# Optimization experiments

Hardware: AMD Instinct MI355X
Metric: run time of the kernel (lower is better)

The kernel has to match this reference:

```python
import jax, jax.numpy as jnp
import numpy as np

L1 = 0.5  # link length 1 (module-level torch.Tensor([0.5]))
L2 = 0.5  # link length 2
SIZE = 8388608
N_MULTS = 1  # len(mul_approx_func_arr)
EPS = 1e-6


def setup_inputs() -> dict:
    key = jax.random.key(0)
    k1, k2 = jax.random.split(key)
    inp = jax.random.normal(k1, (1, SIZE, 2), dtype=jnp.float32)
    # nn.Parameter init: np.tile([1,1,1,1]*100, (n_mults,1)) -> all 100.0
    weight = jnp.ones((N_MULTS, 4), dtype=jnp.float32) * 100.0
    return {"input": inp, "weight": weight}


def _st_clamp(a, lo, hi):
    # value = clamp(a, lo, hi); gradient = identity (matches torch data-swap + hardtanh)
    return a + jax.lax.stop_gradient(jnp.clip(a, lo, hi) - a)


def _forward(inp, weight):
    x = inp[0, :, 0]  # (SIZE,)
    y = inp[0, :, 1]  # (SIZE,)
    outs = []
    for ii in range(weight.shape[0]):  # loop over small fixed n_mults
        w = weight[ii]
        # QuantizeGrad: round+clamp forward, straight-through gradient
        c = w + jax.lax.stop_gradient(jnp.clip(jnp.round(w), 0.001, None) - w)
        xs = x * c[0]
        ys = y * c[1]
        l1s = L1 * c[2]
        l2s = L2 * c[3]
        # --- approx branch (defines forward VALUES; mul_wrapper ~= exact mul) ---
        dis = xs * xs + ys * ys + EPS
        t2a = jnp.arccos(jnp.clip((dis - l1s * l1s - l2s * l2s) / (2.0 * l1s * l2s + EPS), -1.0, 1.0))
        t1a = jnp.arcsin(jnp.clip((ys * (l1s + l2s * jnp.cos(t2a)) - xs * l2s * jnp.sin(t2a)) / dis, -1.0, 1.0))
        approx_res = jnp.stack([t1a, t2a], axis=-1)  # (SIZE, 2)
        # --- grad branch (defines GRADIENT path) ---
        arg2 = (xs * xs + ys * ys - l1s * l1s - l2s * l2s) / (2.0 * l1s * l2s + 1.0)
        t2g = jnp.arccos(_st_clamp(arg2, -0.999, 0.999))
        arg1 = (ys * (l1s + l2s * jnp.cos(t2g)) - xs * l2s * jnp.sin(t2g)) / (xs * xs + ys * ys + 1.0)
        t1g = jnp.arcsin(_st_clamp(arg1, -0.999, 0.999))
        grad_res = jnp.stack([t1g, t2g], axis=-1)  # (SIZE, 2)
        # straight-through: forward value from approx, backward through grad branch
        out_ii = grad_res + jax.lax.stop_gradient(approx_res - grad_res)
        outs.append(out_ii[None, :, :])  # (1, SIZE, 2)
    return jnp.stack(outs, axis=0)  # (N_MULTS, 1, SIZE, 2)


def reference(input, weight):
    return _forward(input, weight)
```

## Files before the change

### kernel.cpp

```cpp
#include <hip/hip_runtime.h>

__device__ __forceinline__ float poly_p(float a) {
    return fmaf(a, fmaf(a, fmaf(a, -0.0187293f, 0.0742610f), -0.2121144f),
                1.5707288f);
}

__device__ __forceinline__ float fast_acos(float x) {
    float a = fabsf(x);
    float r = sqrtf(fmaxf(1.0f - a, 0.0f)) * poly_p(a);
    return x >= 0.0f ? r : 3.14159265f - r;
}

__device__ __forceinline__ float fast_asin(float x) {
    float a = fabsf(x);
    float r = 1.5707963f - sqrtf(fmaxf(1.0f - a, 0.0f)) * poly_p(a);
    return copysignf(r, x);
}

__device__ __forceinline__ void ik_solve(float x, float y,
                                         float c0, float c1,
                                         float l1s, float l2s,
                                         float sumsq, float rden,
                                         float& t1, float& t2) {
    float xs = x * c0;
    float ys = y * c1;
    float dis = fmaf(xs, xs, fmaf(ys, ys, 1e-6f));
    float arg = (dis - sumsq) * rden;
    arg = fminf(fmaxf(arg, -1.0f), 1.0f);
    t2 = fast_acos(arg);
    float st2 = sqrtf(fmaxf(fmaf(-arg, arg, 1.0f), 0.0f));
    float num = ys * fmaf(l2s, arg, l1s) - xs * l2s * st2;
    float a1 = num * __builtin_amdgcn_rcpf(dis);
    a1 = fminf(fmaxf(a1, -1.0f), 1.0f);
    t1 = fast_asin(a1);
}

__global__ __launch_bounds__(256)
void Forward_Model_27616639714074_kernel(const float* __restrict__ in,
                                         const float* __restrict__ w,
                                         float* __restrict__ out,
                                         long long n,
                                         int n_mults) {
    long long tid = (long long)blockIdx.x * blockDim.x + threadIdx.x;
    long long stride = (long long)gridDim.x * blockDim.x;
    long long n4 = n >> 2;

    for (int ii = 0; ii < n_mults; ++ii) {
        float c0  = fmaxf(rintf(w[ii * 4 + 0]), 0.001f);
        float c1  = fmaxf(rintf(w[ii * 4 + 1]), 0.001f);
        float l1s = 0.5f * fmaxf(rintf(w[ii * 4 + 2]), 0.001f);
        float l2s = 0.5f * fmaxf(rintf(w[ii * 4 + 3]), 0.001f);
        float sumsq = l1s * l1s + l2s * l2s;
        float rden  = 1.0f / (2.0f * l1s * l2s + 1e-6f);
        float* outp = out + (long long)ii * n;

        const float4* in4 = reinterpret_cast<const float4*>(in);
        float4* out4 = reinterpret_cast<float4*>(outp);

        #pragma unroll 2
        for (long long i = tid; i < n4; i += stride) {
            float4 v = in4[i];
            float4 r;
            ik_solve(v.x, v.y, c0, c1, l1s, l2s, sumsq, rden, r.x, r.y);
            ik_solve(v.z, v.w, c0, c1, l1s, l2s, sumsq, rden, r.z, r.w);
            out4[i] = r;
        }

        long long pair_start = (n4 << 2) >> 1;
        long long n_pairs = n >> 1;
        for (long long p = pair_start + tid; p < n_pairs; p += stride) {
            float x = in[p * 2 + 0];
            float y = in[p * 2 + 1];
            float t1, t2;
            ik_solve(x, y, c0, c1, l1s, l2s, sumsq, rden, t1, t2);
            outp[p * 2 + 0] = t1;
            outp[p * 2 + 1] = t2;
        }
    }
}

extern "C" void kernel_launch(void* const* d_in, const int* in_sizes, int n_in,
                              void* d_out, int out_size, void* d_ws, size_t ws_size,
                              hipStream_t stream) {
    const float* in = (const float*)d_in[0];
    const float* w  = (const float*)d_in[1];
    float* out = (float*)d_out;

    long long n = in_sizes[0];
    int n_mults = in_sizes[1] / 4;

    int block = 256;
    long long n4 = n >> 2;
    long long want = (n4 + block - 1) / block;
    int grid = (int)(want < 2048 ? (want > 0 ? want : 1) : 2048);

    Forward_Model_27616639714074_kernel<<<grid, block, 0, stream>>>(
        in, w, out, n, n_mults);
}
```

Before: 27.23 us.

## Split into prep kernel plus one-element-per-thread nontemporal main kernel

Moves the weight quantization and derived constants into a tiny prep kernel that writes them to workspace. The grid-stride loop is replaced by a flat one-float4-per-thread kernel with 32-bit indexing, and loads and stores use nontemporal builtins. Odd tails go to a separate tail kernel. This adds an extra kernel launch and a dependent read of the constants buffer in exchange for a simpler main loop and streaming memory hints.

```diff
diff --git a/kernel.cpp b/kernel.cpp
--- a/kernel.cpp
+++ b/kernel.cpp
@@ -1,4 +1,6 @@
 #include <hip/hip_runtime.h>
+
+typedef float f32x4 __attribute__((ext_vector_type(4)));
 
 __device__ __forceinline__ float poly_p(float a) {
     return fmaf(a, fmaf(a, fmaf(a, -0.0187293f, 0.0742610f), -0.2121144f),
@@ -35,48 +37,54 @@
     t1 = fast_asin(a1);
 }
 
+__global__ void Forward_Model_27616639714074_prep(const float* __restrict__ w,
+                                                  float* __restrict__ cbuf,
+                                                  int n_mults) {
+    int ii = threadIdx.x;
+    if (ii >= n_mults) return;
+    float c0  = fmaxf(rintf(w[ii * 4 + 0]), 0.001f);
+    float c1  = fmaxf(rintf(w[ii * 4 + 1]), 0.001f);
+    float l1s = 0.5f * fmaxf(rintf(w[ii * 4 + 2]), 0.001f);
+    float l2s = 0.5f * fmaxf(rintf(w[ii * 4 + 3]), 0.001f);
+    cbuf[ii * 6 + 0] = c0;
+    cbuf[ii * 6 + 1] = c1;
+    cbuf[ii * 6 + 2] = l1s;
+    cbuf[ii * 6 + 3] = l2s;
+    cbuf[ii * 6 + 4] = l1s * l1s + l2s * l2s;
+    cbuf[ii * 6 + 5] = 1.0f / (2.0f * l1s * l2s + 1e-6f);
+}
+
 __global__ __launch_bounds__(256)
-void Forward_Model_27616639714074_kernel(const float* __restrict__ in,
-                                         const float* __restrict__ w,
+void Forward_Model_27616639714074_kernel_c(const f32x4* __restrict__ in4,
+                                           f32x4* __restrict__ out4,
+                                           const float* __restrict__ cbuf,
+                                           unsigned int n4) {
+    float c0 = cbuf[0], c1 = cbuf[1], l1s = cbuf[2], l2s = cbuf[3];
+    float sumsq = cbuf[4], rden = cbuf[5];
+    unsigned int i = blockIdx.x * 256u + threadIdx.x;
+    if (i >= n4) return;
+    f32x4 v = __builtin_nontemporal_load(&in4[i]);
+    f32x4 r;
+    float r0, r1, r2, r3;
+    ik_solve(v.x, v.y, c0, c1, l1s, l2s, sumsq, rden, r0, r1);
+    ik_solve(v.z, v.w, c0, c1, l1s, l2s, sumsq, rden, r2, r3);
+    r.x = r0; r.y = r1; r.z = r2; r.w = r3;
+    __builtin_nontemporal_store(r, &out4[i]);
+}
+
+__global__ __launch_bounds__(64)
+void Forward_Model_27616639714074_tail_c(const float* __restrict__ in,
                                          float* __restrict__ out,
-                                         long long n,
-                                         int n_mults) {
-    long long tid = (long long)blockIdx.x * blockDim.x + threadIdx.x;
-    long long stride = (long long)gridDim.x * blockDim.x;
-    long long n4 = n >> 2;
-
-    for (int ii = 0; ii < n_mults; ++ii) {
-        float c0  = fmaxf(rintf(w[ii * 4 + 0]), 0.001f);
-        float c1  = fmaxf(rintf(w[ii * 4 + 1]), 0.001f);
-        float l1s = 0.5f * fmaxf(rintf(w[ii * 4 + 2]), 0.001f);
-        float l2s = 0.5f * fmaxf(rintf(w[ii * 4 + 3]), 0.001f);
-        float sumsq = l1s * l1s + l2s * l2s;
-        float rden  = 1.0f / (2.0f * l1s * l2s + 1e-6f);
-        float* outp = out + (long long)ii * n;
-
-        const float4* in4 = reinterpret_cast<const float4*>(in);
-        float4* out4 = reinterpret_cast<float4*>(outp);
-
-        #pragma unroll 2
-        for (long long i = tid; i < n4; i += stride) {
-            float4 v = in4[i];
-            float4 r;
-            ik_solve(v.x, v.y, c0, c1, l1s, l2s, sumsq, rden, r.x, r.y);
-            ik_solve(v.z, v.w, c0, c1, l1s, l2s, sumsq, rden, r.z, r.w);
-            out4[i] = r;
-        }
-
-        long long pair_start = (n4 << 2) >> 1;
-        long long n_pairs = n >> 1;
-        for (long long p = pair_start + tid; p < n_pairs; p += stride) {
-            float x = in[p * 2 + 0];
-            float y = in[p * 2 + 1];
-            float t1, t2;
-            ik_solve(x, y, c0, c1, l1s, l2s, sumsq, rden, t1, t2);
-            outp[p * 2 + 0] = t1;
-            outp[p * 2 + 1] = t2;
-        }
-    }
+                                         const float* __restrict__ cbuf,
+                                         long long pair_start, long long n_pairs) {
+    float c0 = cbuf[0], c1 = cbuf[1], l1s = cbuf[2], l2s = cbuf[3];
+    float sumsq = cbuf[4], rden = cbuf[5];
+    long long p = pair_start + blockIdx.x * 64 + threadIdx.x;
+    if (p >= n_pairs) return;
+    float t1, t2;
+    ik_solve(in[p * 2 + 0], in[p * 2 + 1], c0, c1, l1s, l2s, sumsq, rden, t1, t2);
+    out[p * 2 + 0] = t1;
+    out[p * 2 + 1] = t2;
 }
 
 extern "C" void kernel_launch(void* const* d_in, const int* in_sizes, int n_in,
@@ -85,15 +93,28 @@
     const float* in = (const float*)d_in[0];
     const float* w  = (const float*)d_in[1];
     float* out = (float*)d_out;
+    float* cbuf = (float*)d_ws;
 
     long long n = in_sizes[0];
     int n_mults = in_sizes[1] / 4;
 
-    int block = 256;
-    long long n4 = n >> 2;
-    long long want = (n4 + block - 1) / block;
-    int grid = (int)(want < 2048 ? (want > 0 ? want : 1) : 2048);
+    Forward_Model_27616639714074_prep<<<1, 64, 0, stream>>>(w, cbuf, n_mults);
 
-    Forward_Model_27616639714074_kernel<<<grid, block, 0, stream>>>(
-        in, w, out, n, n_mults);
+    unsigned int n4 = (unsigned int)(n >> 2);
+    unsigned int grid = (n4 + 255u) / 256u;
+    long long pair_start = ((long long)n4 << 2) >> 1;
+    long long n_pairs = n >> 1;
+    long long tail_pairs = n_pairs - pair_start;
+
+    for (int ii = 0; ii < n_mults; ++ii) {
+        const f32x4* in4 = reinterpret_cast<const f32x4*>(in);
+        f32x4* out4 = reinterpret_cast<f32x4*>(out + (long long)ii * n);
+        Forward_Model_27616639714074_kernel_c<<<grid, 256, 0, stream>>>(
+            in4, out4, cbuf + ii * 6, n4);
+        if (tail_pairs > 0) {
+            unsigned int tgrid = (unsigned int)((tail_pairs + 63) / 64);
+            Forward_Model_27616639714074_tail_c<<<tgrid, 64, 0, stream>>>(
+                in, out + (long long)ii * n, cbuf + ii * 6, pair_start, n_pairs);
+        }
+    }
 }
```

After: 32.06 us. +17.7%, slower.
